# Kernel tuning notes

Hardware: AMD Instinct MI355X
Metric: run time of the kernel (lower is better)

## Reference

```python
import jax, jax.numpy as jnp
import numpy as np

BS = 256      # number of graphs
NODES = 128   # nodes per graph (equal-size segments)
N = BS * NODES
D = 64        # node feature dim
C = 64        # codebook atoms
K = 32        # support points per atom


def setup_inputs() -> dict:
    key = jax.random.key(0)
    k1, k2 = jax.random.split(key)
    x = jax.random.normal(k1, (N, D), dtype=jnp.float32)
    atoms = jax.random.normal(k2, (C, K, D), dtype=jnp.float32)
    batch = jnp.repeat(jnp.arange(BS, dtype=jnp.int64), NODES)  # sorted graph ids
    return {"x": x, "atoms": atoms, "batch": batch, "bs": BS}


def _sq_dists(a, b):
    # a: [..., n, D], b: [..., m, D] -> [..., n, m] squared euclidean distances
    an = jnp.sum(a * a, axis=-1)
    bn = jnp.sum(b * b, axis=-1)
    ab = jnp.einsum('...nd,...md->...nm', a, b)
    return an[..., :, None] + bn[..., None, :] - 2.0 * ab


def reference(x, atoms, batch, bs):
    # Faithful vectorized version of GINSWDSingleModel._mmd_distances with
    # gamma = 1/D (default). Assumes equal-size graphs (batch = repeat(arange(bs), n)).
    Nn, Dd = x.shape
    Cc, Kk, _ = atoms.shape
    n = Nn // bs
    gamma = 1.0 / Dd
    xg = x.reshape(bs, n, Dd)                      # [bs, n, D]

    # k_xx: within-graph RBF kernel mean, per graph -> [bs]
    k_xx = jnp.exp(-gamma * _sq_dists(xg, xg)).mean(axis=(1, 2))

    # k_yy: within-atom kernel mean, per atom -> [C]
    k_yy = jnp.exp(-gamma * _sq_dists(atoms, atoms)).mean(axis=(1, 2))

    # k_xy: cross kernel mean between graph nodes and atom points -> [bs, C]
    xn = jnp.sum(xg * xg, axis=-1)                 # [bs, n]
    an = jnp.sum(atoms * atoms, axis=-1)           # [C, K]
    xa = jnp.einsum('bnd,ckd->bnck', xg, atoms)    # [bs, n, C, K]
    dxy = xn[:, :, None, None] + an[None, None, :, :] - 2.0 * xa
    k_xy = jnp.exp(-gamma * dxy).mean(axis=(1, 3))  # [bs, C]

    return k_xx[:, None] + k_yy[None, :] - 2.0 * k_xy
```

## Files before the change

### kernel.cpp

```cpp
#include <hip/hip_runtime.h>
#include <hip/hip_bf16.h>


constexpr int   NODES = 128;
constexpr int   DD    = 64;
constexpr int   CC    = 64;
constexpr int   KK    = 32;
constexpr float GAMMA = 1.0f / 64.0f;
constexpr float LOG2E = 1.4426950408889634f;
constexpr float C1    = 2.0f * GAMMA * LOG2E;
constexpr float GL    = GAMMA * LOG2E;

typedef __attribute__((ext_vector_type(8)))  short short8;
typedef __attribute__((ext_vector_type(16))) float f32x16;

#define MFMA(a, b, c) __builtin_amdgcn_mfma_f32_32x32x16_bf16((a), (b), (c), 0, 0, 0)

__device__ __forceinline__ float fexp2(float x) {
    float r;
    asm("v_exp_f32 %0, %1" : "=v"(r) : "v"(x));
    return r;
}

__device__ __forceinline__ unsigned short f2bf(float f) {
    union { float f; unsigned int u; } a; a.f = f;
    unsigned int u = a.u;
    return (unsigned short)((u + 0x7FFFu + ((u >> 16) & 1u)) >> 16);
}

__device__ __forceinline__ void gl16(const void* g, void* l) {
    __builtin_amdgcn_global_load_lds(
        (const __attribute__((address_space(1))) char*)g,
        (__attribute__((address_space(3))) char*)l, 16, 0, 0);
}

__global__ __launch_bounds__(256) void prep(const float* __restrict__ x,
                                            const float* __restrict__ atoms,
                                            short8* __restrict__ xfrag,
                                            float* __restrict__ nrm,
                                            short8* __restrict__ bfrag,
                                            float* __restrict__ eck,
                                            float* __restrict__ kyy) {
    __shared__ float smem[NODES * (DD + 1)];
    const int bid = blockIdx.x, t = threadIdx.x;

    if (bid < 256) {
        const int b = bid;
        float (*a)[DD + 1] = (float(*)[DD + 1])smem;

        const float4* xg = reinterpret_cast<const float4*>(x + (size_t)b * NODES * DD);
        for (int i = t; i < NODES * DD / 4; i += 256) {
            const float4 v = xg[i];
            const int r = i >> 4, c4 = (i & 15) * 4;
            a[r][c4 + 0] = v.x; a[r][c4 + 1] = v.y;
            a[r][c4 + 2] = v.z; a[r][c4 + 3] = v.w;
        }
        __syncthreads();

        if (t < NODES) {
            float s = 0.f;
#pragma unroll
            for (int d = 0; d < DD; ++d) s = fmaf(a[t][d], a[t][d], s);
            nrm[b * NODES + t] = -GL * s;
        }
#pragma unroll
        for (int j = 0; j < 4; ++j) {
            const int e = t + 256 * j;
            const int l = e & 63, sl = e >> 6;
            const int row = (sl >> 2) * 32 + (l & 31);
            const int k0  = (sl & 3) * 16 + (l >> 5) * 8;
            short8 h;
#pragma unroll
            for (int q = 0; q < 8; ++q) h[q] = (short)f2bf(a[row][k0 + q]);
            xfrag[(size_t)b * 1024 + e] = h;
        }
    } else {
        const int c = bid - 256;
        float (*a)[DD + 1] = (float(*)[DD + 1])smem;
        float* an   = smem + KK * (DD + 1);
        float* wred = an + KK;

        const float* ac = atoms + (size_t)c * KK * DD;
        for (int i = t; i < KK * DD; i += 256) a[i >> 6][i & 63] = ac[i];
        __syncthreads();

        if (t < KK) {
            float s = 0.f;
#pragma unroll
            for (int d = 0; d < DD; ++d) s = fmaf(a[t][d], a[t][d], s);
            an[t] = s;
            eck[c * KK + t] = fexp2(-GL * s);
        }
        __syncthreads();

        {
            const int wv = t >> 6, l = t & 63;
            const int kp = l & 31, khh = l >> 5;
            short8 h;
#pragma unroll
            for (int j = 0; j < 8; ++j) h[j] = (short)f2bf(a[kp][wv * 16 + khh * 8 + j]);
            bfrag[(size_t)c * 256 + wv * 64 + l] = h;
        }

        {
            const int i = t >> 3, j0 = (t & 7) * 4;
            float s0 = 0, s1 = 0, s2 = 0, s3 = 0;
            for (int d = 0; d < DD; ++d) {
                const float aid = a[i][d];
                s0 = fmaf(aid, a[j0 + 0][d], s0);
                s1 = fmaf(aid, a[j0 + 1][d], s1);
                s2 = fmaf(aid, a[j0 + 2][d], s2);
                s3 = fmaf(aid, a[j0 + 3][d], s3);
            }
            const float ani = an[i];
            float s = fexp2(-GL * (ani + an[j0 + 0] - 2.f * s0))
                    + fexp2(-GL * (ani + an[j0 + 1] - 2.f * s1))
                    + fexp2(-GL * (ani + an[j0 + 2] - 2.f * s2))
                    + fexp2(-GL * (ani + an[j0 + 3] - 2.f * s3));
#pragma unroll
            for (int off = 32; off; off >>= 1) s += __shfl_xor(s, off);
            if ((t & 63) == 0) wred[t >> 6] = s;
        }
        __syncthreads();
        if (t == 0) kyy[c] = (wred[0] + wred[1] + wred[2] + wred[3]) * (1.0f / (KK * KK));
    }
}

__global__ __launch_bounds__(256, 4) void mmd_fused(const short8* __restrict__ xfrag,
                                                    const short8* __restrict__ bfrag,
                                                    const float* __restrict__ nrm,
                                                    const float* __restrict__ eck,
                                                    float* __restrict__ kxxp,
                                                    float* __restrict__ sxyw) {
    const int bid = blockIdx.x, b = bid >> 2, cq = bid & 3;
    const int t = threadIdx.x, w = t >> 6, l = t & 63;
    const int l31 = l & 31, kh = l >> 5, rh = w >> 1, aq = w & 1;

    __shared__ short8 Bb[2][4][256];
    __shared__ short8 Bx[256];
    __shared__ float  part16[4][9][16];
    __shared__ float  nl[NODES];

    const short8* xa = xfrag + (size_t)b * 1024;
    short8 A0[4], A1[4];
#pragma unroll
    for (int kt = 0; kt < 4; ++kt) {
        A0[kt] = xa[((2 * rh) * 4 + kt) * 64 + l];
        A1[kt] = xa[((2 * rh + 1) * 4 + kt) * 64 + l];
    }

    if (t < NODES) nl[t] = nrm[b * NODES + t];

    float ecv[8];
#pragma unroll
    for (int j = 0; j < 8; ++j)
        ecv[j] = eck[(cq * 16 + aq * 8 + j) * KK + l31];

    gl16(xa + ((size_t)cq * 4 + w) * 64 + l, &Bx[w * 64]);
    __syncthreads();

    const float ec0 = fexp2(nl[cq * 32 + l31]);
    const float* nbase = &nl[(2 * rh) * 32 + 4 * kh];
    const short8* bq = bfrag + (size_t)(cq * 16) * 256;

#pragma unroll
    for (int s = 0; s <= 4; ++s) {
        if (s < 4) {
            const int ct = (w >> 1) * 8 + 2 * s + (w & 1);
            const short8* src = bq + (size_t)ct * 256;
#pragma unroll
            for (int q = 0; q < 4; ++q)
                gl16(src + q * 64 + l, &Bb[s & 1][w][q * 64]);
        }

        if (s == 0) {
            short8 Bt[4];
#pragma unroll
            for (int kt = 0; kt < 4; ++kt) Bt[kt] = Bx[kt * 64 + l];
            f32x16 acc = {};
            if (aq == 0) {
#pragma unroll
                for (int kt = 0; kt < 4; ++kt) acc = MFMA(A0[kt], Bt[kt], acc);
            } else {
#pragma unroll
                for (int kt = 0; kt < 4; ++kt) acc = MFMA(A1[kt], Bt[kt], acc);
            }
            float ssum = 0.f;
            const float* nb = &nl[(2 * rh + aq) * 32 + 4 * kh];
#pragma unroll
            for (int q = 0; q < 4; ++q) {
                const float4 cn = *reinterpret_cast<const float4*>(nb + 8 * q);
                ssum += fexp2(fmaf(C1, acc[4 * q + 0], cn.x));
                ssum += fexp2(fmaf(C1, acc[4 * q + 1], cn.y));
                ssum += fexp2(fmaf(C1, acc[4 * q + 2], cn.z));
                ssum += fexp2(fmaf(C1, acc[4 * q + 3], cn.w));
            }
            ssum *= ec0;
            ssum += __shfl_xor(ssum, 32);
            ssum += __shfl_xor(ssum, 16);
            if (l < 16) part16[w][8][l] = ssum;
        } else {
            const int set = s - 1, buf = set & 1;
#pragma unroll
            for (int p = 0; p < 2; ++p) {
                short8 Bt[4];
#pragma unroll
                for (int kt = 0; kt < 4; ++kt)
                    Bt[kt] = Bb[buf][aq * 2 + p][kt * 64 + l];
                f32x16 a0 = {}, a1 = {};
#pragma unroll
                for (int kt = 0; kt < 4; ++kt) {
                    a0 = MFMA(A0[kt], Bt[kt], a0);
                    a1 = MFMA(A1[kt], Bt[kt], a1);
                }
                float sA = 0.f, sB = 0.f;
#pragma unroll
                for (int q = 0; q < 4; ++q) {
                    const float4 cA = *reinterpret_cast<const float4*>(nbase + 8 * q);
                    const float4 cB = *reinterpret_cast<const float4*>(nbase + 32 + 8 * q);
                    sA += fexp2(fmaf(C1, a0[4 * q + 0], cA.x));
                    sA += fexp2(fmaf(C1, a0[4 * q + 1], cA.y));
                    sA += fexp2(fmaf(C1, a0[4 * q + 2], cA.z));
                    sA += fexp2(fmaf(C1, a0[4 * q + 3], cA.w));
                    sB += fexp2(fmaf(C1, a1[4 * q + 0], cB.x));
                    sB += fexp2(fmaf(C1, a1[4 * q + 1], cB.y));
                    sB += fexp2(fmaf(C1, a1[4 * q + 2], cB.z));
                    sB += fexp2(fmaf(C1, a1[4 * q + 3], cB.w));
                }
                float ssum = (sA + sB) * ecv[2 * set + p];
                ssum += __shfl_xor(ssum, 32);
                ssum += __shfl_xor(ssum, 16);
                if (l < 16) part16[w][2 * set + p][l] = ssum;
            }
        }
        __syncthreads();
    }

    {
        const int o = t >> 4, g = t & 15;
        const int aqo = o >> 3, ito = o & 7;
        float s = part16[aqo][ito][g] + part16[2 + aqo][ito][g];
        s += __shfl_xor(s, 8);
        s += __shfl_xor(s, 4);
        s += __shfl_xor(s, 2);
        s += __shfl_xor(s, 1);
        if (g == 0) sxyw[b * CC + cq * 16 + aqo * 8 + ito] = s;
    }
    if (t < 16) {
        float s = part16[0][8][t] + part16[1][8][t]
                + part16[2][8][t] + part16[3][8][t];
        s += __shfl_xor(s, 8);
        s += __shfl_xor(s, 4);
        s += __shfl_xor(s, 2);
        s += __shfl_xor(s, 1);
        if (t == 0) kxxp[b * 4 + cq] = s;
    }
}

__global__ __launch_bounds__(256) void combine(const float* __restrict__ kxxp,
                                               const float* __restrict__ kyy,
                                               const float* __restrict__ sxyw,
                                               float* __restrict__ out) {
    const int idx = blockIdx.x * 256 + threadIdx.x;
    const int b = idx >> 6, c = idx & 63;
    const float kxx = (kxxp[b * 4 + 0] + kxxp[b * 4 + 1] +
                       kxxp[b * 4 + 2] + kxxp[b * 4 + 3]) * (1.0f / 16384.0f);
    out[idx] = kxx + kyy[c] - sxyw[idx] * (1.0f / 2048.0f);
}

extern "C" void kernel_launch(void* const* d_in, const int* in_sizes, int n_in,
                              void* d_out, int out_size, void* d_ws, size_t ws_size,
                              hipStream_t stream) {
    const float* x     = (const float*)d_in[0];
    const float* atoms = (const float*)d_in[1];
    float* out = (float*)d_out;

    char* ws = (char*)d_ws;
    short8* xfrag = (short8*)(ws);
    short8* bfrag = (short8*)(ws + 4194304);
    float*  nrm   = (float*) (ws + 4456448);
    float*  eck   = (float*) (ws + 4587520);
    float*  kyy   = (float*) (ws + 4595712);
    float*  kxxp  = (float*) (ws + 4595968);
    float*  sxyw  = (float*) (ws + 4600064);

    prep      <<<dim3(320),  dim3(256), 0, stream>>>(x, atoms, xfrag, nrm, bfrag, eck, kyy);
    mmd_fused <<<dim3(1024), dim3(256), 0, stream>>>(xfrag, bfrag, nrm, eck, kxxp, sxyw);
    combine   <<<dim3(CC),   dim3(256), 0, stream>>>(kxxp, kyy, sxyw, out);
}
```

Measured before the change: 29.52 us.

## Fold norm biases into MFMA accumulator init and pre-scale atom fragments

```diff
diff --git a/kernel.cpp b/kernel.cpp
--- a/kernel.cpp
+++ b/kernel.cpp
@@ -17,9 +17,11 @@
 #define MFMA(a, b, c) __builtin_amdgcn_mfma_f32_32x32x16_bf16((a), (b), (c), 0, 0, 0)
 
 __device__ __forceinline__ float fexp2(float x) {
-    float r;
-    asm("v_exp_f32 %0, %1" : "=v"(r) : "v"(x));
-    return r;
+#if __has_builtin(__builtin_amdgcn_exp2f)
+    return __builtin_amdgcn_exp2f(x);
+#else
+    return exp2f(x);
+#endif
 }
 
 __device__ __forceinline__ unsigned short f2bf(float f) {
@@ -39,7 +41,7 @@
                                             short8* __restrict__ xfrag,
                                             float* __restrict__ nrm,
                                             short8* __restrict__ bfrag,
-                                            float* __restrict__ eck,
+                                            float* __restrict__ can,
                                             float* __restrict__ kyy) {
     __shared__ float smem[NODES * (DD + 1)];
     const int bid = blockIdx.x, t = threadIdx.x;
@@ -89,7 +91,7 @@
 #pragma unroll
             for (int d = 0; d < DD; ++d) s = fmaf(a[t][d], a[t][d], s);
             an[t] = s;
-            eck[c * KK + t] = fexp2(-GL * s);
+            can[c * KK + t] = -GL * s;
         }
         __syncthreads();
 
@@ -98,7 +100,8 @@
             const int kp = l & 31, khh = l >> 5;
             short8 h;
 #pragma unroll
-            for (int j = 0; j < 8; ++j) h[j] = (short)f2bf(a[kp][wv * 16 + khh * 8 + j]);
+            for (int j = 0; j < 8; ++j)
+                h[j] = (short)f2bf(C1 * a[kp][wv * 16 + khh * 8 + j]);
             bfrag[(size_t)c * 256 + wv * 64 + l] = h;
         }
 
@@ -129,108 +132,92 @@
 __global__ __launch_bounds__(256, 4) void mmd_fused(const short8* __restrict__ xfrag,
                                                     const short8* __restrict__ bfrag,
                                                     const float* __restrict__ nrm,
-                                                    const float* __restrict__ eck,
+                                                    const float* __restrict__ can,
                                                     float* __restrict__ kxxp,
                                                     float* __restrict__ sxyw) {
     const int bid = blockIdx.x, b = bid >> 2, cq = bid & 3;
     const int t = threadIdx.x, w = t >> 6, l = t & 63;
-    const int l31 = l & 31, kh = l >> 5, rh = w >> 1, aq = w & 1;
+    const int l31 = l & 31, kh = l >> 5;
 
     __shared__ short8 Bb[2][4][256];
-    __shared__ short8 Bx[256];
-    __shared__ float  part16[4][9][16];
-    __shared__ float  nl[NODES];
+    __shared__ float  part16[4][17][16];
 
     const short8* xa = xfrag + (size_t)b * 1024;
-    short8 A0[4], A1[4];
-#pragma unroll
-    for (int kt = 0; kt < 4; ++kt) {
-        A0[kt] = xa[((2 * rh) * 4 + kt) * 64 + l];
-        A1[kt] = xa[((2 * rh + 1) * 4 + kt) * 64 + l];
-    }
-
-    if (t < NODES) nl[t] = nrm[b * NODES + t];
-
-    float ecv[8];
-#pragma unroll
-    for (int j = 0; j < 8; ++j)
-        ecv[j] = eck[(cq * 16 + aq * 8 + j) * KK + l31];
-
-    gl16(xa + ((size_t)cq * 4 + w) * 64 + l, &Bx[w * 64]);
+    short8 A[4];
+#pragma unroll
+    for (int kt = 0; kt < 4; ++kt) A[kt] = xa[(w * 4 + kt) * 64 + l];
+
+    f32x16 cx;
+    {
+        const float* nb = nrm + b * NODES + w * 32 + 4 * kh;
+#pragma unroll
+        for (int q = 0; q < 4; ++q) {
+            const float4 v = *reinterpret_cast<const float4*>(nb + 8 * q);
+            cx[4*q+0] = v.x; cx[4*q+1] = v.y; cx[4*q+2] = v.z; cx[4*q+3] = v.w;
+        }
+    }
+    float cav[16];
+#pragma unroll
+    for (int j = 0; j < 16; ++j) cav[j] = can[(cq * 16 + j) * KK + l31];
+
+    const float ec0 = fexp2(nrm[b * NODES + cq * 32 + l31]);
+    const short8* bq = bfrag + (size_t)(cq * 16) * 256;
+
+    {
+        const short8* src = (w == 0) ? (xa + cq * 256) : (bq + (size_t)(w - 1) * 256);
+#pragma unroll
+        for (int q = 0; q < 4; ++q) gl16(src + q * 64 + l, &Bb[0][w][q * 64]);
+    }
     __syncthreads();
 
-    const float ec0 = fexp2(nl[cq * 32 + l31]);
-    const float* nbase = &nl[(2 * rh) * 32 + 4 * kh];
-    const short8* bq = bfrag + (size_t)(cq * 16) * 256;
-
-#pragma unroll
-    for (int s = 0; s <= 4; ++s) {
+#pragma unroll
+    for (int s = 0; s < 5; ++s) {
         if (s < 4) {
-            const int ct = (w >> 1) * 8 + 2 * s + (w & 1);
-            const short8* src = bq + (size_t)ct * 256;
-#pragma unroll
-            for (int q = 0; q < 4; ++q)
-                gl16(src + q * 64 + l, &Bb[s & 1][w][q * 64]);
-        }
-
-        if (s == 0) {
-            short8 Bt[4];
-#pragma unroll
-            for (int kt = 0; kt < 4; ++kt) Bt[kt] = Bx[kt * 64 + l];
-            f32x16 acc = {};
-            if (aq == 0) {
-#pragma unroll
-                for (int kt = 0; kt < 4; ++kt) acc = MFMA(A0[kt], Bt[kt], acc);
-            } else {
-#pragma unroll
-                for (int kt = 0; kt < 4; ++kt) acc = MFMA(A1[kt], Bt[kt], acc);
+            const int g = 4 * (s + 1) + w;
+            if (g <= 16) {
+                const short8* src = bq + (size_t)(g - 1) * 256;
+#pragma unroll
+                for (int q = 0; q < 4; ++q)
+                    gl16(src + q * 64 + l, &Bb[(s + 1) & 1][w][q * 64]);
             }
-            float ssum = 0.f;
-            const float* nb = &nl[(2 * rh + aq) * 32 + 4 * kh];
-#pragma unroll
-            for (int q = 0; q < 4; ++q) {
-                const float4 cn = *reinterpret_cast<const float4*>(nb + 8 * q);
-                ssum += fexp2(fmaf(C1, acc[4 * q + 0], cn.x));
-                ssum += fexp2(fmaf(C1, acc[4 * q + 1], cn.y));
-                ssum += fexp2(fmaf(C1, acc[4 * q + 2], cn.z));
-                ssum += fexp2(fmaf(C1, acc[4 * q + 3], cn.w));
-            }
-            ssum *= ec0;
-            ssum += __shfl_xor(ssum, 32);
-            ssum += __shfl_xor(ssum, 16);
-            if (l < 16) part16[w][8][l] = ssum;
-        } else {
-            const int set = s - 1, buf = set & 1;
-#pragma unroll
-            for (int p = 0; p < 2; ++p) {
+        }
+#pragma unroll
+        for (int p = 0; p < 4; ++p) {
+            const int g = 4 * s + p;
+            if (g <= 16) {
                 short8 Bt[4];
 #pragma unroll
-                for (int kt = 0; kt < 4; ++kt)
-                    Bt[kt] = Bb[buf][aq * 2 + p][kt * 64 + l];
-                f32x16 a0 = {}, a1 = {};
-#pragma unroll
-                for (int kt = 0; kt < 4; ++kt) {
-                    a0 = MFMA(A0[kt], Bt[kt], a0);
-                    a1 = MFMA(A1[kt], Bt[kt], a1);
+                for (int kt = 0; kt < 4; ++kt) Bt[kt] = Bb[s & 1][p][kt * 64 + l];
+
+                float ssum;
+                if (g == 0) {
+                    f32x16 acc = {};
+#pragma unroll
+                    for (int kt = 0; kt < 4; ++kt) acc = MFMA(A[kt], Bt[kt], acc);
+                    float sa = 0.f, sb = 0.f;
+#pragma unroll
+                    for (int r = 0; r < 16; r += 2) {
+                        sa += fexp2(fmaf(C1, acc[r],     cx[r]));
+                        sb += fexp2(fmaf(C1, acc[r + 1], cx[r + 1]));
+                    }
+                    ssum = (sa + sb) * ec0;
+                } else {
+                    f32x16 acc;
+#pragma unroll
+                    for (int r = 0; r < 16; ++r) acc[r] = cx[r] + cav[g - 1];
+#pragma unroll
+                    for (int kt = 0; kt < 4; ++kt) acc = MFMA(A[kt], Bt[kt], acc);
+                    float sa = 0.f, sb = 0.f;
+#pragma unroll
+                    for (int r = 0; r < 16; r += 2) {
+                        sa += fexp2(acc[r]);
+                        sb += fexp2(acc[r + 1]);
+                    }
+                    ssum = sa + sb;
                 }
-                float sA = 0.f, sB = 0.f;
-#pragma unroll
-                for (int q = 0; q < 4; ++q) {
-                    const float4 cA = *reinterpret_cast<const float4*>(nbase + 8 * q);
-                    const float4 cB = *reinterpret_cast<const float4*>(nbase + 32 + 8 * q);
-                    sA += fexp2(fmaf(C1, a0[4 * q + 0], cA.x));
-                    sA += fexp2(fmaf(C1, a0[4 * q + 1], cA.y));
-                    sA += fexp2(fmaf(C1, a0[4 * q + 2], cA.z));
-                    sA += fexp2(fmaf(C1, a0[4 * q + 3], cA.w));
-                    sB += fexp2(fmaf(C1, a1[4 * q + 0], cB.x));
-                    sB += fexp2(fmaf(C1, a1[4 * q + 1], cB.y));
-                    sB += fexp2(fmaf(C1, a1[4 * q + 2], cB.z));
-                    sB += fexp2(fmaf(C1, a1[4 * q + 3], cB.w));
-                }
-                float ssum = (sA + sB) * ecv[2 * set + p];
                 ssum += __shfl_xor(ssum, 32);
                 ssum += __shfl_xor(ssum, 16);
-                if (l < 16) part16[w][2 * set + p][l] = ssum;
+                if (l < 16) part16[w][g][l] = ssum;
             }
         }
         __syncthreads();
@@ -238,17 +225,17 @@
 
     {
         const int o = t >> 4, g = t & 15;
-        const int aqo = o >> 3, ito = o & 7;
-        float s = part16[aqo][ito][g] + part16[2 + aqo][ito][g];
+        float s = part16[0][o + 1][g] + part16[1][o + 1][g]
+                + part16[2][o + 1][g] + part16[3][o + 1][g];
         s += __shfl_xor(s, 8);
         s += __shfl_xor(s, 4);
         s += __shfl_xor(s, 2);
         s += __shfl_xor(s, 1);
-        if (g == 0) sxyw[b * CC + cq * 16 + aqo * 8 + ito] = s;
+        if (g == 0) sxyw[b * CC + cq * 16 + o] = s;
     }
     if (t < 16) {
-        float s = part16[0][8][t] + part16[1][8][t]
-                + part16[2][8][t] + part16[3][8][t];
+        float s = part16[0][0][t] + part16[1][0][t]
+                + part16[2][0][t] + part16[3][0][t];
         s += __shfl_xor(s, 8);
         s += __shfl_xor(s, 4);
         s += __shfl_xor(s, 2);
@@ -279,12 +266,12 @@
     short8* xfrag = (short8*)(ws);
     short8* bfrag = (short8*)(ws + 4194304);
     float*  nrm   = (float*) (ws + 4456448);
-    float*  eck   = (float*) (ws + 4587520);
+    float*  can   = (float*) (ws + 4587520);
     float*  kyy   = (float*) (ws + 4595712);
     float*  kxxp  = (float*) (ws + 4595968);
     float*  sxyw  = (float*) (ws + 4600064);
 
-    prep      <<<dim3(320),  dim3(256), 0, stream>>>(x, atoms, xfrag, nrm, bfrag, eck, kyy);
-    mmd_fused <<<dim3(1024), dim3(256), 0, stream>>>(xfrag, bfrag, nrm, eck, kxxp, sxyw);
+    prep      <<<dim3(320),  dim3(256), 0, stream>>>(x, atoms, xfrag, nrm, bfrag, can, kyy);
+    mmd_fused <<<dim3(1024), dim3(256), 0, stream>>>(xfrag, bfrag, nrm, can, kxxp, sxyw);
     combine   <<<dim3(CC),   dim3(256), 0, stream>>>(kxxp, kyy, sxyw, out);
 }
```

Measured after the change: 29.62 us. Within noise of the previous version (+0.3%).
